# Kernel tuning notes

Measured on AMD Instinct MI355X. Metric: run time of the kernel, lower is better.

Reference implementation:

```python
import jax, jax.numpy as jnp
import numpy as np

D = 512   # block_hidden_dim (also per-head dim in this module)
H = 8     # n_head
EPS_RENORM = 1e-13
LN_EPS = 1e-5

def setup_inputs() -> dict:
    key = jax.random.key(0)
    ks = jax.random.split(key, 10)
    B, L = 4, 1024
    std = np.sqrt(2.0 / (D * 2)).astype(np.float32)
    q = jax.random.normal(ks[0], (B, L, D), jnp.float32)
    k = jax.random.normal(ks[1], (B, L, D), jnp.float32)
    v = jax.random.normal(ks[2], (B, L, D), jnp.float32)
    mask = jax.random.randint(ks[3], (B, L, L), 0, 2, jnp.int32)
    Wq = jax.random.normal(ks[4], (H * D, D), jnp.float32) * std
    Wk = jax.random.normal(ks[5], (H * D, D), jnp.float32) * std
    Wv = jax.random.normal(ks[6], (H * D, D), jnp.float32) * std
    Wfc = jax.random.normal(ks[7], (D, H * D), jnp.float32) * np.sqrt(2.0 / (D + H * D)).astype(np.float32)
    bfc = jnp.zeros((D,), jnp.float32)
    gamma = jnp.ones((D,), jnp.float32)
    beta = jnp.zeros((D,), jnp.float32)
    return {"q": q, "mask": mask, "k": k, "v": v, "Wq": Wq, "Wk": Wk,
            "Wv": Wv, "Wfc": Wfc, "bfc": bfc, "gamma": gamma, "beta": beta}

def reference(q, mask, k, v, Wq, Wk, Wv, Wfc, bfc, gamma, beta):
    B, Lq, _ = q.shape
    residual = q
    # torch Linear: y = x @ W.T ; W reshaped to [H, D_out, D_in]
    qh = jnp.einsum('bqd,hed->bhqe', q, Wq.reshape(H, D, D))
    kh = jnp.einsum('bkd,hed->bhke', k, Wk.reshape(H, D, D))
    vh = jnp.einsum('bkd,hed->bhke', v, Wv.reshape(H, D, D))
    scores = jnp.einsum('bhqe,bhke->bhqk', qh, kh) / jnp.sqrt(jnp.float32(D))
    m = mask.astype(scores.dtype)[:, None, :, :]        # [B,1,Lq,Lk]
    # multiplicative-mask softmax + renormalization (allennlp masked_softmax)
    attn = jax.nn.softmax(scores * m, axis=-1)
    attn = attn * m
    attn = attn / (attn.sum(axis=-1, keepdims=True) + EPS_RENORM)
    out = jnp.einsum('bhqk,bhke->bhqe', attn, vh)       # [B,H,Lq,D]
    out = out.transpose(0, 2, 1, 3).reshape(B, Lq, H * D)  # head-major concat
    out = out @ Wfc.T + bfc                              # fc (dropout = eval no-op)
    x = out + residual
    mu = x.mean(axis=-1, keepdims=True)
    var = x.var(axis=-1, keepdims=True)
    out = (x - mu) / jnp.sqrt(var + LN_EPS) * gamma + beta
    attn_mean = attn.mean(axis=1)                        # mean over heads [B,Lq,Lk]
    return out, attn_mean
```

## Files before the change

### kernel.cpp

```cpp
#include <hip/hip_runtime.h>
#include <hip/hip_bf16.h>
#include <cmath>

typedef long long i64;
typedef unsigned short u16;
typedef __attribute__((ext_vector_type(8))) short short8;
typedef __attribute__((ext_vector_type(8))) unsigned short u16x8;
typedef __attribute__((ext_vector_type(4))) float f32x4;

#define NB 4
#define NL 1024
#define ND 512
#define NH 8

__device__ __forceinline__ u16 f2bf(float f) {
    __hip_bfloat16 h = __float2bfloat16(f);
    return __builtin_bit_cast(unsigned short, h);
}
__device__ __forceinline__ float bf2f(u16 u) {
    return __builtin_bit_cast(float, (unsigned)u << 16);
}

typedef __attribute__((address_space(3))) u16* lds_u16p;
typedef const __attribute__((address_space(1))) u16* glb_u16p;
__device__ __forceinline__ void gl_lds16(const u16* g, u16* l) {
    __builtin_amdgcn_global_load_lds((glb_u16p)g, (lds_u16p)l, 16, 0, 0);
}

struct CvtArgs {
    const float* src[4];
    u16* dst[4];
};

__global__ __launch_bounds__(256) void cvt_multi_kernel(CvtArgs args, int n8)
{
    int i = blockIdx.x * 256 + threadIdx.x;
    if (i >= n8) return;
    const float* __restrict__ src = args.src[blockIdx.y];
    u16* __restrict__ dst = args.dst[blockIdx.y];
    float4 a = ((const float4*)src)[2 * i];
    float4 b = ((const float4*)src)[2 * i + 1];
    u16x8 o;
    o[0] = f2bf(a.x); o[1] = f2bf(a.y); o[2] = f2bf(a.z); o[3] = f2bf(a.w);
    o[4] = f2bf(b.x); o[5] = f2bf(b.y); o[6] = f2bf(b.z); o[7] = f2bf(b.w);
    *(u16x8*)&dst[8 * i] = o;
}

template <bool OUTBF, bool BIAS>
__global__ __launch_bounds__(256) void mfma_gemm(
    const u16* __restrict__ A, const u16* __restrict__ B,
    void* __restrict__ Cv, const float* __restrict__ bias,
    int K, int lda, int ldb, int ldc, float alpha,
    i64 a_s1, i64 a_s2, i64 b_s1, i64 b_s2, i64 c_s1, i64 c_s2)
{
    const int gxy  = gridDim.x * gridDim.y;
    const int nblk = gxy * gridDim.z;
    const int lin  = blockIdx.x + gridDim.x * blockIdx.y + gxy * blockIdx.z;
    const int swz  = (lin & 7) * (nblk >> 3) + (lin >> 3);
    const int bz   = swz / gxy;
    const int rxy  = swz - bz * gxy;
    const int by   = rxy / gridDim.x;
    const int bx   = rxy - by * gridDim.x;

    const int zh = bz >> 3, zl = bz & 7;
    A += (i64)zh * a_s1 + (i64)zl * a_s2;
    B += (i64)zh * b_s1 + (i64)zl * b_s2;
    const i64 coff = (i64)zh * c_s1 + (i64)zl * c_s2;

    __shared__ alignas(16) u16 As[128 * 64];
    __shared__ alignas(16) u16 Bs[128 * 64];

    const int tid  = threadIdx.x;
    const int lane = tid & 63;
    const int wave = tid >> 6;
    const int wr   = (wave >> 1) * 64;
    const int wc   = (wave & 1) * 64;
    const int lrow = lane & 15;
    const int kblk = lane >> 4;
    const int rsw  = (lrow & 7) * 8;
    const int m0   = by * 128;
    const int n0   = bx * 128;

    const int srow0 = wave * 32;
    const int lrel  = lane >> 3;
    const int grow  = srow0 + lrel;
    const int gchk  = ((lane & 7) ^ lrel) * 8;

    f32x4 acc[4][4];
    #pragma unroll
    for (int i = 0; i < 4; ++i)
        #pragma unroll
        for (int j = 0; j < 4; ++j)
            acc[i][j] = (f32x4){0.f, 0.f, 0.f, 0.f};

    for (int k0 = 0; k0 < K; k0 += 64) {
        #pragma unroll
        for (int j = 0; j < 4; ++j)
            gl_lds16(&A[(i64)(m0 + grow + 8 * j) * lda + k0 + gchk],
                     &As[(srow0 + 8 * j) * 64]);
        #pragma unroll
        for (int j = 0; j < 4; ++j)
            gl_lds16(&B[(i64)(n0 + grow + 8 * j) * ldb + k0 + gchk],
                     &Bs[(srow0 + 8 * j) * 64]);
        __syncthreads();

        #pragma unroll
        for (int kk = 0; kk < 2; ++kk) {
            short8 af[4], bg[4];
            #pragma unroll
            for (int m = 0; m < 4; ++m)
                af[m] = *(const short8*)&As[(wr + m * 16 + lrow) * 64 +
                                            (((kk * 32) + kblk * 8) ^ rsw)];
            #pragma unroll
            for (int n = 0; n < 4; ++n)
                bg[n] = *(const short8*)&Bs[(wc + n * 16 + lrow) * 64 +
                                            (((kk * 32) + kblk * 8) ^ rsw)];

            #pragma unroll
            for (int m = 0; m < 4; ++m)
                #pragma unroll
                for (int n = 0; n < 4; ++n)
                    acc[m][n] = __builtin_amdgcn_mfma_f32_16x16x32_bf16(
                        af[m], bg[n], acc[m][n], 0, 0, 0);
        }
        __syncthreads();
    }

    #pragma unroll
    for (int m = 0; m < 4; ++m) {
        #pragma unroll
        for (int n = 0; n < 4; ++n) {
            const int col = n0 + wc + n * 16 + lrow;
            float bv = BIAS ? bias[col] : 0.f;
            #pragma unroll
            for (int r = 0; r < 4; ++r) {
                const int row = m0 + wr + m * 16 + kblk * 4 + r;
                float val = acc[m][n][r] * alpha + bv;
                if (OUTBF)
                    ((u16*)Cv)[coff + (i64)row * ldc + col] = f2bf(val);
                else
                    ((float*)Cv)[coff + (i64)row * ldc + col] = val;
            }
        }
    }
}

template <int P>
__global__ __launch_bounds__(256) void reduce_fc_kernel(
    const float* __restrict__ part, const float* __restrict__ bias,
    float* __restrict__ outp, i64 pstride)
{
    i64 idx = (i64)blockIdx.x * 256 + threadIdx.x;
    float s = bias[idx & (ND - 1)];
    #pragma unroll
    for (int p = 0; p < P; ++p) s += part[(i64)p * pstride + idx];
    outp[idx] = s;
}

__device__ __forceinline__ float wave_red_sum(float v) {
    #pragma unroll
    for (int o = 32; o > 0; o >>= 1) v += __shfl_down(v, o, 64);
    return v;
}
__device__ __forceinline__ float wave_red_max(float v) {
    #pragma unroll
    for (int o = 32; o > 0; o >>= 1) v = fmaxf(v, __shfl_down(v, o, 64));
    return v;
}

__global__ __launch_bounds__(256) void softmax_fused_kernel(
    const u16* __restrict__ scores, const int* __restrict__ mask,
    u16* __restrict__ attn_bf, float* __restrict__ amean,
    i64 s_bstride, i64 m_bstride, i64 a_bstride, i64 o_bstride)
{
    const int qrow = blockIdx.x;
    const int bb   = blockIdx.y;
    const u16* sbase = scores + (i64)bb * s_bstride;
    const int* mrow = mask + (i64)bb * m_bstride + (i64)qrow * NL;
    u16* abase = attn_bf + (i64)bb * a_bstride;
    float* orow = amean + (i64)bb * o_bstride + (i64)qrow * NL;

    const int tid  = threadIdx.x;
    const int lane = tid & 63, wid = tid >> 6;
    __shared__ float red[4];

    float mv[4];
    #pragma unroll
    for (int i = 0; i < 4; ++i) mv[i] = (float)mrow[tid + i * 256];

    float msum[4] = {0.f, 0.f, 0.f, 0.f};

    for (int h = 0; h < NH; ++h) {
        const u16* srow_p = sbase + ((i64)h * NL + qrow) * NL;
        u16* arow_p = abase + ((i64)h * NL + qrow) * NL;

        float zv[4];
        float lmax = -1e30f;
        #pragma unroll
        for (int i = 0; i < 4; ++i) {
            zv[i] = bf2f(srow_p[tid + i * 256]) * mv[i];
            lmax = fmaxf(lmax, zv[i]);
        }
        float wv = wave_red_max(lmax);
        __syncthreads();
        if (lane == 0) red[wid] = wv;
        __syncthreads();
        const float gmax = fmaxf(fmaxf(red[0], red[1]), fmaxf(red[2], red[3]));

        float e[4];
        float ls = 0.f;
        #pragma unroll
        for (int i = 0; i < 4; ++i) { e[i] = __expf(zv[i] - gmax); ls += e[i]; }
        wv = wave_red_sum(ls);
        __syncthreads();
        if (lane == 0) red[wid] = wv;
        __syncthreads();
        const float S1 = red[0] + red[1] + red[2] + red[3];

        float ls2 = 0.f;
        #pragma unroll
        for (int i = 0; i < 4; ++i) { e[i] = e[i] / S1 * mv[i]; ls2 += e[i]; }
        wv = wave_red_sum(ls2);
        __syncthreads();
        if (lane == 0) red[wid] = wv;
        __syncthreads();
        const float S2 = red[0] + red[1] + red[2] + red[3];

        const float inv = 1.0f / (S2 + 1e-13f);
        #pragma unroll
        for (int i = 0; i < 4; ++i) {
            float p = e[i] * inv;
            arow_p[tid + i * 256] = f2bf(p);
            msum[i] += p;
        }
    }

    #pragma unroll
    for (int i = 0; i < 4; ++i)
        orow[tid + i * 256] = msum[i] * 0.125f;
}

__global__ __launch_bounds__(256) void ln_kernel(
    const float* __restrict__ fcout, const float* __restrict__ resid,
    const float* __restrict__ gamma, const float* __restrict__ beta,
    float* __restrict__ out)
{
    const int row = blockIdx.x;
    const float* xr = fcout + (i64)row * ND;
    const float* rr = resid + (i64)row * ND;
    const int tid = threadIdx.x;
    const int lane = tid & 63, wid = tid >> 6;
    __shared__ float red[8];

    float x0 = xr[tid] + rr[tid];
    float x1 = xr[tid + 256] + rr[tid + 256];
    float s  = x0 + x1;
    float s2 = x0 * x0 + x1 * x1;
    s  = wave_red_sum(s);
    s2 = wave_red_sum(s2);
    if (lane == 0) { red[wid] = s; red[4 + wid] = s2; }
    __syncthreads();
    const float S  = red[0] + red[1] + red[2] + red[3];
    const float S2 = red[4] + red[5] + red[6] + red[7];
    const float mu  = S * (1.0f / ND);
    const float var = S2 * (1.0f / ND) - mu * mu;
    const float inv = rsqrtf(var + 1e-5f);

    out[(i64)row * ND + tid]       = (x0 - mu) * inv * gamma[tid] + beta[tid];
    out[(i64)row * ND + tid + 256] = (x1 - mu) * inv * gamma[tid + 256] + beta[tid + 256];
}

template <bool BT, bool BIAS, bool ACC>
__global__ __launch_bounds__(256) void gemm_kernel(
    const float* __restrict__ A, const float* __restrict__ B,
    float* __restrict__ C, const float* __restrict__ bias,
    int M, int N, int K, int lda, int ldb, int ldc, float alpha)
{
    __shared__ float Asf[16][68];
    __shared__ float Bsf[16][68];
    const int tid = threadIdx.x;
    const int tx = tid & 15, ty = tid >> 4;
    const int m0 = blockIdx.y * 64, n0 = blockIdx.x * 64;
    float acc[4][4] = {};

    for (int k0 = 0; k0 < K; k0 += 16) {
        {
            int r = tid >> 2, kq = (tid & 3) << 2;
            float4 a = *reinterpret_cast<const float4*>(&A[(i64)(m0 + r) * lda + k0 + kq]);
            Asf[kq][r] = a.x; Asf[kq + 1][r] = a.y; Asf[kq + 2][r] = a.z; Asf[kq + 3][r] = a.w;
        }
        if (BT) {
            int r = tid >> 2, kq = (tid & 3) << 2;
            float4 b = *reinterpret_cast<const float4*>(&B[(i64)(n0 + r) * ldb + k0 + kq]);
            Bsf[kq][r] = b.x; Bsf[kq + 1][r] = b.y; Bsf[kq + 2][r] = b.z; Bsf[kq + 3][r] = b.w;
        } else {
            int kk = tid >> 4, n4 = (tid & 15) << 2;
            float4 b = *reinterpret_cast<const float4*>(&B[(i64)(k0 + kk) * ldb + n0 + n4]);
            *reinterpret_cast<float4*>(&Bsf[kk][n4]) = b;
        }
        __syncthreads();
        #pragma unroll
        for (int kk = 0; kk < 16; ++kk) {
            float4 a4 = *reinterpret_cast<const float4*>(&Asf[kk][ty << 2]);
            float4 b4 = *reinterpret_cast<const float4*>(&Bsf[kk][tx << 2]);
            float a[4] = {a4.x, a4.y, a4.z, a4.w};
            float b[4] = {b4.x, b4.y, b4.z, b4.w};
            #pragma unroll
            for (int i = 0; i < 4; ++i)
                #pragma unroll
                for (int j = 0; j < 4; ++j)
                    acc[i][j] = fmaf(a[i], b[j], acc[i][j]);
        }
        __syncthreads();
    }
    #pragma unroll
    for (int i = 0; i < 4; ++i) {
        int m = m0 + (ty << 2) + i;
        #pragma unroll
        for (int j = 0; j < 4; ++j) {
            int n = n0 + (tx << 2) + j;
            float val = acc[i][j] * alpha;
            if (BIAS) val += bias[n];
            i64 idx = (i64)m * ldc + n;
            if (ACC) C[idx] += val; else C[idx] = val;
        }
    }
}

__global__ __launch_bounds__(256) void softmax_kernel(
    float* __restrict__ attn, const int* __restrict__ mask)
{
    const int qrow = blockIdx.x;
    float* row = attn + (i64)qrow * NL;
    const int* mrow = mask + (i64)qrow * NL;
    const int tid = threadIdx.x;
    const int lane = tid & 63, wid = tid >> 6;
    __shared__ float red[4];

    float zv[4], mv[4];
    float lmax = -1e30f;
    #pragma unroll
    for (int i = 0; i < 4; ++i) {
        mv[i] = (float)mrow[tid + i * 256];
        zv[i] = row[tid + i * 256] * mv[i];
        lmax  = fmaxf(lmax, zv[i]);
    }
    float wv = wave_red_max(lmax);
    if (lane == 0) red[wid] = wv;
    __syncthreads();
    const float gmax = fmaxf(fmaxf(red[0], red[1]), fmaxf(red[2], red[3]));
    float e[4]; float ls = 0.f;
    #pragma unroll
    for (int i = 0; i < 4; ++i) { e[i] = __expf(zv[i] - gmax); ls += e[i]; }
    __syncthreads();
    wv = wave_red_sum(ls);
    if (lane == 0) red[wid] = wv;
    __syncthreads();
    const float S1 = red[0] + red[1] + red[2] + red[3];
    float ls2 = 0.f;
    #pragma unroll
    for (int i = 0; i < 4; ++i) { e[i] = e[i] / S1 * mv[i]; ls2 += e[i]; }
    __syncthreads();
    wv = wave_red_sum(ls2);
    if (lane == 0) red[wid] = wv;
    __syncthreads();
    const float S2 = red[0] + red[1] + red[2] + red[3];
    const float inv = 1.0f / (S2 + 1e-13f);
    #pragma unroll
    for (int i = 0; i < 4; ++i) row[tid + i * 256] = e[i] * inv;
}

__global__ __launch_bounds__(256) void mean_acc_kernel(
    const float* __restrict__ attn, float* __restrict__ out, int first)
{
    i64 idx = (i64)blockIdx.x * 256 + threadIdx.x;
    float v = attn[idx] * 0.125f;
    out[idx] = first ? v : (out[idx] + v);
}

extern "C" void kernel_launch(void* const* d_in, const int* in_sizes, int n_in,
                              void* d_out, int out_size, void* d_ws, size_t ws_size,
                              hipStream_t stream)
{
    const float* q     = (const float*)d_in[0];
    const int*   mask  = (const int*)  d_in[1];
    const float* k     = (const float*)d_in[2];
    const float* v     = (const float*)d_in[3];
    const float* Wq    = (const float*)d_in[4];
    const float* Wk    = (const float*)d_in[5];
    const float* Wv    = (const float*)d_in[6];
    const float* Wfc   = (const float*)d_in[7];
    const float* bfc   = (const float*)d_in[8];
    const float* gamma = (const float*)d_in[9];
    const float* beta  = (const float*)d_in[10];

    float* out       = (float*)d_out;
    float* attn_mean = out + (i64)NB * NL * ND;

    const float inv_sqrt_d = 0.04419417382415922f;
    const i64 LD  = (i64)NL * ND;
    const i64 LL  = (i64)NL * NL;
    const i64 ND2 = (i64)ND * ND;
    const i64 HLD = (i64)NH * LD;
    const i64 HLL = (i64)NH * LL;
    dim3 blk(256);

    const size_t MB = 1048576;

    if (ws_size >= 196 * MB) {
        char* wsb = (char*)d_ws;
        u16* Wq_bf  = (u16*)(wsb);
        u16* Wk_bf  = (u16*)(wsb + 4   * MB);
        u16* Wv_bf  = (u16*)(wsb + 8   * MB);
        u16* Wfc_bf = (u16*)(wsb + 12  * MB);
        u16* q_bf   = (u16*)(wsb + 16  * MB);
        u16* k_bf   = (u16*)(wsb + 20  * MB);
        u16* v_bf   = (u16*)(wsb + 24  * MB);
        u16* qh     = (u16*)(wsb + 28  * MB);
        u16* kh     = (u16*)(wsb + 60  * MB);
        u16* vht    = (u16*)(wsb + 92  * MB);
        u16* scores = (u16*)(wsb + 124 * MB);
        u16* attn_bf  = qh;
        u16* concat   = (u16*)(wsb + 124 * MB);
        float* fcpart = (float*)(wsb + 156 * MB);
        float* fcout  = (float*)(wsb + 188 * MB);

        {
            CvtArgs a;
            a.src[0] = Wq;  a.dst[0] = Wq_bf;
            a.src[1] = Wk;  a.dst[1] = Wk_bf;
            a.src[2] = Wv;  a.dst[2] = Wv_bf;
            a.src[3] = Wfc; a.dst[3] = Wfc_bf;
            cvt_multi_kernel<<<dim3(1024, 4), blk, 0, stream>>>(a, 262144);
        }
        {
            CvtArgs a;
            a.src[0] = q; a.dst[0] = q_bf;
            a.src[1] = k; a.dst[1] = k_bf;
            a.src[2] = v; a.dst[2] = v_bf;
            a.src[3] = q; a.dst[3] = q_bf;
            cvt_multi_kernel<<<dim3(1024, 3), blk, 0, stream>>>(a, 262144);
        }

        mfma_gemm<true, false><<<dim3(4, 8, 32), blk, 0, stream>>>(
            q_bf, Wq_bf, qh, nullptr, ND, ND, ND, ND, 1.0f,
            LD, 0, 0, ND2, HLD, LD);
        mfma_gemm<true, false><<<dim3(4, 8, 32), blk, 0, stream>>>(
            k_bf, Wk_bf, kh, nullptr, ND, ND, ND, ND, 1.0f,
            LD, 0, 0, ND2, HLD, LD);
        mfma_gemm<true, false><<<dim3(8, 4, 32), blk, 0, stream>>>(
            Wv_bf, v_bf, vht, nullptr, ND, ND, ND, NL, 1.0f,
            0, ND2, LD, 0, HLD, LD);

        mfma_gemm<true, false><<<dim3(8, 8, 32), blk, 0, stream>>>(
            qh, kh, scores, nullptr, ND, ND, ND, NL, inv_sqrt_d,
            HLD, LD, HLD, LD, HLL, LL);

        softmax_fused_kernel<<<dim3(NL, NB), blk, 0, stream>>>(
            scores, mask, attn_bf, attn_mean, HLL, LL, HLL, LL);

        mfma_gemm<true, false><<<dim3(4, 8, 32), blk, 0, stream>>>(
            attn_bf, vht, concat, nullptr, NL, NL, NL, NH * ND, 1.0f,
            HLL, LL, HLD, LD, (i64)NL * NH * ND, (i64)ND);

        mfma_gemm<false, false><<<dim3(4, 32, 4), blk, 0, stream>>>(
            concat, Wfc_bf, fcpart, nullptr, NL, NH * ND, NH * ND, ND, 1.0f,
            0, NL, 0, NL, 0, (i64)NB * NL * ND);
        reduce_fc_kernel<4><<<dim3(8192), blk, 0, stream>>>(
            fcpart, bfc, fcout, (i64)NB * NL * ND);

        ln_kernel<<<dim3(NB * NL), blk, 0, stream>>>(fcout, q, gamma, beta, out);

    } else if (ws_size >= 64 * MB) {
        char* wsb = (char*)d_ws;
        u16* Wq_bf  = (u16*)(wsb);
        u16* Wk_bf  = (u16*)(wsb + 4  * MB);
        u16* Wv_bf  = (u16*)(wsb + 8  * MB);
        u16* Wfc_bf = (u16*)(wsb + 12 * MB);
        u16* qb_bf  = (u16*)(wsb + 16 * MB);
        u16* kb_bf  = (u16*)(wsb + 17 * MB);
        u16* vb_bf  = (u16*)(wsb + 18 * MB);
        u16* qh     = (u16*)(wsb + 19 * MB);
        u16* kh     = (u16*)(wsb + 27 * MB);
        u16* vht    = (u16*)(wsb + 35 * MB);
        u16* scores = (u16*)(wsb + 43 * MB);
        u16* attn_bf  = qh;
        u16* concat   = (u16*)(wsb + 43 * MB);
        float* fcpart = (float*)(wsb + 51 * MB);
        float* fcout  = (float*)(wsb + 59 * MB);

        {
            CvtArgs a;
            a.src[0] = Wq;  a.dst[0] = Wq_bf;
            a.src[1] = Wk;  a.dst[1] = Wk_bf;
            a.src[2] = Wv;  a.dst[2] = Wv_bf;
            a.src[3] = Wfc; a.dst[3] = Wfc_bf;
            cvt_multi_kernel<<<dim3(1024, 4), blk, 0, stream>>>(a, 262144);
        }

        for (int b = 0; b < NB; ++b) {
            const float* qb = q + (i64)b * LD;
            const float* kb = k + (i64)b * LD;
            const float* vb = v + (i64)b * LD;
            const int* maskb = mask + (i64)b * LL;

            {
                CvtArgs a;
                a.src[0] = qb; a.dst[0] = qb_bf;
                a.src[1] = kb; a.dst[1] = kb_bf;
                a.src[2] = vb; a.dst[2] = vb_bf;
                a.src[3] = vb; a.dst[3] = vb_bf;
                cvt_multi_kernel<<<dim3(256, 3), blk, 0, stream>>>(a, 65536);
            }

            mfma_gemm<true, false><<<dim3(4, 8, NH), blk, 0, stream>>>(
                qb_bf, Wq_bf, qh, nullptr, ND, ND, ND, ND, 1.0f,
                0, 0, 0, ND2, 0, LD);
            mfma_gemm<true, false><<<dim3(4, 8, NH), blk, 0, stream>>>(
                kb_bf, Wk_bf, kh, nullptr, ND, ND, ND, ND, 1.0f,
                0, 0, 0, ND2, 0, LD);
            mfma_gemm<true, false><<<dim3(8, 4, NH), blk, 0, stream>>>(
                Wv_bf, vb_bf, vht, nullptr, ND, ND, ND, NL, 1.0f,
                0, ND2, 0, 0, 0, LD);

            mfma_gemm<true, false><<<dim3(8, 8, NH), blk, 0, stream>>>(
                qh, kh, scores, nullptr, ND, ND, ND, NL, inv_sqrt_d,
                0, LD, 0, LD, 0, LL);

            softmax_fused_kernel<<<dim3(NL, 1), blk, 0, stream>>>(
                scores, maskb, attn_bf, attn_mean + (i64)b * LL, 0, 0, 0, 0);

            mfma_gemm<true, false><<<dim3(4, 8, NH), blk, 0, stream>>>(
                attn_bf, vht, concat, nullptr, NL, NL, NL, NH * ND, 1.0f,
                0, LL, 0, LD, 0, (i64)ND);

            mfma_gemm<false, false><<<dim3(4, 8, 4), blk, 0, stream>>>(
                concat, Wfc_bf, fcpart, nullptr, NL, NH * ND, NH * ND, ND, 1.0f,
                0, NL, 0, NL, 0, LD);
            reduce_fc_kernel<4><<<dim3(2048), blk, 0, stream>>>(fcpart, bfc, fcout, LD);

            ln_kernel<<<dim3(NL), blk, 0, stream>>>(fcout, qb, gamma, beta, out + (i64)b * LD);
        }
    } else {
        float* ws = (float*)d_ws;
        float* qh_h   = ws;
        float* kh_h   = ws + LD;
        float* vh_h   = ws + 2 * LD;
        float* attn_h = ws + 3 * LD;
        float* headout = qh_h;
        float* fcout   = ws + 5 * LD;

        for (int b = 0; b < NB; ++b) {
            const float* qb = q + (i64)b * LD;
            const float* kb = k + (i64)b * LD;
            const float* vb = v + (i64)b * LD;
            const int* maskb = mask + (i64)b * LL;

            for (int h = 0; h < NH; ++h) {
                const i64 wofs = (i64)h * ND2;
                gemm_kernel<true, false, false><<<dim3(8, 16, 1), blk, 0, stream>>>(
                    qb, Wq + wofs, qh_h, nullptr, NL, ND, ND, ND, ND, ND, 1.0f);
                gemm_kernel<true, false, false><<<dim3(8, 16, 1), blk, 0, stream>>>(
                    kb, Wk + wofs, kh_h, nullptr, NL, ND, ND, ND, ND, ND, 1.0f);
                gemm_kernel<true, false, false><<<dim3(8, 16, 1), blk, 0, stream>>>(
                    vb, Wv + wofs, vh_h, nullptr, NL, ND, ND, ND, ND, ND, 1.0f);
                gemm_kernel<true, false, false><<<dim3(16, 16, 1), blk, 0, stream>>>(
                    qh_h, kh_h, attn_h, nullptr, NL, NL, ND, ND, ND, NL, inv_sqrt_d);
                softmax_kernel<<<dim3(NL), blk, 0, stream>>>(attn_h, maskb);
                mean_acc_kernel<<<dim3(4096), blk, 0, stream>>>(
                    attn_h, attn_mean + (i64)b * LL, h == 0 ? 1 : 0);
                gemm_kernel<false, false, false><<<dim3(8, 16, 1), blk, 0, stream>>>(
                    attn_h, vh_h, headout, nullptr, NL, ND, NL, NL, ND, ND, 1.0f);
                if (h == 0)
                    gemm_kernel<true, true, false><<<dim3(8, 16, 1), blk, 0, stream>>>(
                        headout, Wfc + (i64)h * ND, fcout, bfc, NL, ND, ND, ND, NH * ND, ND, 1.0f);
                else
                    gemm_kernel<true, false, true><<<dim3(8, 16, 1), blk, 0, stream>>>(
                        headout, Wfc + (i64)h * ND, fcout, nullptr, NL, ND, ND, ND, NH * ND, ND, 1.0f);
            }
            ln_kernel<<<dim3(NL), blk, 0, stream>>>(fcout, qb, gamma, beta, out + (i64)b * LD);
        }
    }
}
```

Measured before the change: 288.5 us.

## Assign one head per wave in softmax kernel with vectorized loads

The masked softmax kernel now lets each of the four waves own whole head rows (two heads per wave), so the max and sum reductions become wave-local shuffles instead of block-wide reductions with multiple __syncthreads per head. Scores, mask and attention outputs are read and written as 8-element vectors per lane. The per-head mean is combined through a 16 KB shared buffer with a single barrier at the end. This raises register and LDS use per block in exchange for fewer barriers and wider memory transactions.

```diff
diff --git a/kernel.cpp b/kernel.cpp
--- a/kernel.cpp
+++ b/kernel.cpp
@@ -7,6 +7,7 @@
 typedef __attribute__((ext_vector_type(8))) short short8;
 typedef __attribute__((ext_vector_type(8))) unsigned short u16x8;
 typedef __attribute__((ext_vector_type(4))) float f32x4;
+typedef __attribute__((ext_vector_type(4))) int i32x4;
 
 #define NB 4
 #define NL 1024
@@ -181,63 +182,94 @@
     float* orow = amean + (i64)bb * o_bstride + (i64)qrow * NL;
 
     const int tid  = threadIdx.x;
-    const int lane = tid & 63, wid = tid >> 6;
-    __shared__ float red[4];
-
-    float mv[4];
-    #pragma unroll
-    for (int i = 0; i < 4; ++i) mv[i] = (float)mrow[tid + i * 256];
-
-    float msum[4] = {0.f, 0.f, 0.f, 0.f};
-
-    for (int h = 0; h < NH; ++h) {
+    const int lane = tid & 63;
+    const int wave = tid >> 6;
+
+    __shared__ float wsum[4][NL];
+
+    const int e0 = lane * 8;
+    const int e1 = 512 + lane * 8;
+
+    float mv[16];
+    {
+        i32x4 m0a = *(const i32x4*)&mrow[e0];
+        i32x4 m0b = *(const i32x4*)&mrow[e0 + 4];
+        i32x4 m1a = *(const i32x4*)&mrow[e1];
+        i32x4 m1b = *(const i32x4*)&mrow[e1 + 4];
+        #pragma unroll
+        for (int i = 0; i < 4; ++i) {
+            mv[i]      = (float)m0a[i];
+            mv[4 + i]  = (float)m0b[i];
+            mv[8 + i]  = (float)m1a[i];
+            mv[12 + i] = (float)m1b[i];
+        }
+    }
+
+    float msum[16];
+    #pragma unroll
+    for (int i = 0; i < 16; ++i) msum[i] = 0.f;
+
+    #pragma unroll
+    for (int hh = 0; hh < 2; ++hh) {
+        const int h = wave + hh * 4;
         const u16* srow_p = sbase + ((i64)h * NL + qrow) * NL;
         u16* arow_p = abase + ((i64)h * NL + qrow) * NL;
 
-        float zv[4];
+        u16x8 s0 = *(const u16x8*)&srow_p[e0];
+        u16x8 s1 = *(const u16x8*)&srow_p[e1];
+
+        float zv[16];
         float lmax = -1e30f;
         #pragma unroll
-        for (int i = 0; i < 4; ++i) {
-            zv[i] = bf2f(srow_p[tid + i * 256]) * mv[i];
-            lmax = fmaxf(lmax, zv[i]);
-        }
-        float wv = wave_red_max(lmax);
-        __syncthreads();
-        if (lane == 0) red[wid] = wv;
-        __syncthreads();
-        const float gmax = fmaxf(fmaxf(red[0], red[1]), fmaxf(red[2], red[3]));
-
-        float e[4];
+        for (int i = 0; i < 8; ++i) {
+            zv[i]     = bf2f(s0[i]) * mv[i];
+            zv[8 + i] = bf2f(s1[i]) * mv[8 + i];
+        }
+        #pragma unroll
+        for (int i = 0; i < 16; ++i) lmax = fmaxf(lmax, zv[i]);
+        #pragma unroll
+        for (int o = 1; o < 64; o <<= 1)
+            lmax = fmaxf(lmax, __shfl_xor(lmax, o, 64));
+
+        float e[16];
         float ls = 0.f;
         #pragma unroll
-        for (int i = 0; i < 4; ++i) { e[i] = __expf(zv[i] - gmax); ls += e[i]; }
-        wv = wave_red_sum(ls);
-        __syncthreads();
-        if (lane == 0) red[wid] = wv;
-        __syncthreads();
-        const float S1 = red[0] + red[1] + red[2] + red[3];
+        for (int i = 0; i < 16; ++i) { e[i] = __expf(zv[i] - lmax); ls += e[i]; }
+        #pragma unroll
+        for (int o = 1; o < 64; o <<= 1) ls += __shfl_xor(ls, o, 64);
 
         float ls2 = 0.f;
         #pragma unroll
-        for (int i = 0; i < 4; ++i) { e[i] = e[i] / S1 * mv[i]; ls2 += e[i]; }
-        wv = wave_red_sum(ls2);
-        __syncthreads();
-        if (lane == 0) red[wid] = wv;
-        __syncthreads();
-        const float S2 = red[0] + red[1] + red[2] + red[3];
-
-        const float inv = 1.0f / (S2 + 1e-13f);
-        #pragma unroll
-        for (int i = 0; i < 4; ++i) {
-            float p = e[i] * inv;
-            arow_p[tid + i * 256] = f2bf(p);
-            msum[i] += p;
-        }
-    }
-
-    #pragma unroll
-    for (int i = 0; i < 4; ++i)
-        orow[tid + i * 256] = msum[i] * 0.125f;
+        for (int i = 0; i < 16; ++i) { e[i] = e[i] / ls * mv[i]; ls2 += e[i]; }
+        #pragma unroll
+        for (int o = 1; o < 64; o <<= 1) ls2 += __shfl_xor(ls2, o, 64);
+
+        const float inv = 1.0f / (ls2 + 1e-13f);
+        u16x8 o0, o1;
+        #pragma unroll
+        for (int i = 0; i < 8; ++i) {
+            float p0 = e[i] * inv;
+            float p1 = e[8 + i] * inv;
+            o0[i] = f2bf(p0);
+            o1[i] = f2bf(p1);
+            msum[i]     += p0;
+            msum[8 + i] += p1;
+        }
+        *(u16x8*)&arow_p[e0] = o0;
+        *(u16x8*)&arow_p[e1] = o1;
+    }
+
+    #pragma unroll
+    for (int i = 0; i < 8; ++i) {
+        wsum[wave][e0 + i] = msum[i];
+        wsum[wave][e1 + i] = msum[8 + i];
+    }
+    __syncthreads();
+    #pragma unroll
+    for (int i = 0; i < 4; ++i) {
+        int j = tid + i * 256;
+        orow[j] = (wsum[0][j] + wsum[1][j] + wsum[2][j] + wsum[3][j]) * 0.125f;
+    }
 }
 
 __global__ __launch_bounds__(256) void ln_kernel(
```

Result: faster. 272.7 us (-5.5%).
